# Optimization experiments

Measured on AMD Instinct MI355X. Metric: run time of the kernel, lower is better.

## Reference

```python
import jax, jax.numpy as jnp
import numpy as np

S = 4096          # number of samples
N_NODES = 2048    # sum nodes in this layer
N_CHILD = 4096    # nodes per child layer
NNZ = 32768       # nonzeros per sparse log-weight matrix


def setup_inputs() -> dict:
    key = jax.random.key(0)
    ks = jax.random.split(key, 8)
    ll0 = jax.random.normal(ks[0], (S, N_CHILD), dtype=jnp.float32)
    ll1 = jax.random.normal(ks[1], (S, N_CHILD), dtype=jnp.float32)
    w0_data = jax.random.normal(ks[2], (NNZ,), dtype=jnp.float32)
    w1_data = jax.random.normal(ks[3], (NNZ,), dtype=jnp.float32)
    w0_rows = jax.random.randint(ks[4], (NNZ,), 0, N_NODES, dtype=jnp.int32)
    w0_cols = jax.random.randint(ks[5], (NNZ,), 0, N_CHILD, dtype=jnp.int32)
    w1_rows = jax.random.randint(ks[6], (NNZ,), 0, N_NODES, dtype=jnp.int32)
    w1_cols = jax.random.randint(ks[7], (NNZ,), 0, N_CHILD, dtype=jnp.int32)
    return {"ll0": ll0, "ll1": ll1,
            "w0_data": w0_data, "w1_data": w1_data,
            "w0_rows": w0_rows, "w0_cols": w0_cols,
            "w1_rows": w1_rows, "w1_cols": w1_cols,
            "n_nodes": N_NODES}


def _sparse_weighted_sum(ll, data, rows, cols, n_nodes):
    # exp(ll) @ exp(W).T for BCOO W with shape (n_nodes, n_child)
    # contrib[s, k] = exp(ll[s, cols[k]]) * exp(data[k]); scatter-add over rows.
    contrib = jnp.exp(ll[:, cols] + data[None, :])  # (S, NNZ)
    return jnp.zeros((ll.shape[0], n_nodes), dtype=ll.dtype).at[:, rows].add(contrib)


def reference(ll0, ll1, w0_data, w1_data, w0_rows, w0_cols, w1_rows, w1_cols, n_nodes):
    # accumulate exp(ll_i) @ exp(W_i).T over child layers
    result = _sparse_weighted_sum(ll0, w0_data, w0_rows, w0_cols, n_nodes)
    result = result + _sparse_weighted_sum(ll1, w1_data, w1_rows, w1_cols, n_nodes)
    # log normalization constants: log(sum_j exp(concatenated log_weights)[i, j])
    z = jnp.zeros((n_nodes,), dtype=result.dtype)
    z = z.at[w0_rows].add(jnp.exp(w0_data))
    z = z.at[w1_rows].add(jnp.exp(w1_data))
    return jnp.log(result) - jnp.log(z)[None, :]
```

## Files before the change

kernel.cpp:

```cpp
#include <hip/hip_runtime.h>
#include <math.h>

#define S 4096
#define N_NODES 2048
#define N_CHILD 4096
#define NNZ 32768
#define NNZ_TOTAL (2 * NNZ)
#define TSM 512
#define TN 8
#define CAP 96
#define LP 516

typedef float f32x2 __attribute__((ext_vector_type(2)));


__global__ __launch_bounds__(256, 8) void prep_kernel(
        const float* __restrict__ ll0, const float* __restrict__ ll1,
        const float* __restrict__ w0d, const float* __restrict__ w1d,
        const int* __restrict__ w0r, const int* __restrict__ w0c,
        const int* __restrict__ w1r, const int* __restrict__ w1c,
        unsigned char* __restrict__ ET, int2* __restrict__ ent,
        int* __restrict__ counts) {
    __shared__ unsigned int tile[256 * 5];
    int t = threadIdx.x;
    int b = blockIdx.x;
    if (b < 256) {
        int k = b * 256 + t;
        int row, col; float w;
        if (k < NNZ) { row = w0r[k]; col = w0c[k]; w = w0d[k]; }
        else { int kk = k - NNZ; row = w1r[kk]; col = w1c[kk] + N_CHILD; w = w1d[kk]; }
        int pos = atomicAdd(&counts[row], 1);
        if (pos < CAP)
            ent[row * CAP + pos] = make_int2(col, __float_as_int(__expf(w)));
        return;
    }
    int bt = b - 256;
    int slice = bt & 7;
    int ssub = (bt >> 3) & 31;
    int ct = (bt >> 8) & 15;
    int z = (bt >> 12) & 1;
    int s0 = slice * 512 + ssub * 16;
    int c0 = ct * 256;
    const float* ll = z ? ll1 : ll0;
    int wave = t >> 6, lane = t & 63;
    const float* p = ll + (size_t)(s0 + wave * 4) * N_CHILD + c0 + lane * 4;
    float4 a0 = *(const float4*)(p);
    float4 a1 = *(const float4*)(p + N_CHILD);
    float4 a2 = *(const float4*)(p + 2 * N_CHILD);
    float4 a3 = *(const float4*)(p + 3 * N_CHILD);
#pragma unroll
    for (int k = 0; k < 4; ++k) {
        float e0 = __expf(((const float*)&a0)[k]);
        float e1 = __expf(((const float*)&a1)[k]);
        float e2 = __expf(((const float*)&a2)[k]);
        float e3 = __expf(((const float*)&a3)[k]);
        unsigned int wlo = (unsigned int)__builtin_amdgcn_cvt_pk_fp8_f32(
            e0, e1, 0, false);
        unsigned int wfull = (unsigned int)__builtin_amdgcn_cvt_pk_fp8_f32(
            e2, e3, (int)wlo, true);
        tile[(k * 64 + lane) * 5 + wave] = wfull;
    }
    __syncthreads();
    unsigned int d0 = tile[t * 5 + 0];
    unsigned int d1 = tile[t * 5 + 1];
    unsigned int d2 = tile[t * 5 + 2];
    unsigned int d3 = tile[t * 5 + 3];
    int c = (t & 63) * 4 + (t >> 6);
    unsigned char* dst = ET + (size_t)(z * N_CHILD + c0 + c) * S + s0;
    *(uint4*)dst = make_uint4(d0, d1, d2, d3);
}


static __device__ inline void fma16(uint4 x, f32x2 w2, f32x2* a2) {
#pragma unroll
    for (int q = 0; q < 4; ++q) {
        unsigned int word = (q == 0) ? x.x : (q == 1) ? x.y : (q == 2) ? x.z : x.w;
        f32x2 lo = __builtin_amdgcn_cvt_pk_f32_fp8(word, false);
        f32x2 hi = __builtin_amdgcn_cvt_pk_f32_fp8(word, true);
        a2[q * 2 + 0] = lo * w2 + a2[q * 2 + 0];
        a2[q * 2 + 1] = hi * w2 + a2[q * 2 + 1];
    }
}

__global__ __launch_bounds__(256, 8) void main_kernel(
        const unsigned char* __restrict__ ET, const int2* __restrict__ ent,
        const int* __restrict__ counts, float* __restrict__ out) {
    __shared__ float lds[TN * LP];
    int t = threadIdx.x, wave = t >> 6, lane = t & 63;
    int hs = lane >> 5, sl = lane & 31;
    int slice = blockIdx.x & 7;
    int nb = blockIdx.x >> 3;
    int i0 = nb * TN;
    const unsigned char* ETs = ET + slice * TSM + sl * 16;
    for (int jj = 0; jj < 2; ++jj) {
        int j = wave * 2 + jj;
        int i = i0 + j;
        int cnt = __builtin_amdgcn_readfirstlane(counts[i]);
        if (cnt > CAP) cnt = CAP;
        const int2* eb = ent + i * CAP;
        f32x2 a2[8];
#pragma unroll
        for (int u = 0; u < 8; ++u) a2[u] = (f32x2){0.f, 0.f};
        float z = 0.f;
        int n = (cnt + 1 - hs) >> 1;
        int t2 = 0;
        for (; t2 + 1 < n; t2 += 2) {
            int2 e0 = eb[hs + 2 * t2];
            int2 e1 = eb[hs + 2 * t2 + 2];
            uint4 x0 = *(const uint4*)(ETs + (size_t)e0.x * S);
            uint4 x1 = *(const uint4*)(ETs + (size_t)e1.x * S);
            float w0 = __uint_as_float(e0.y);
            float w1 = __uint_as_float(e1.y);
            f32x2 w02 = {w0, w0};
            f32x2 w12 = {w1, w1};
            fma16(x0, w02, a2);
            fma16(x1, w12, a2);
            z += w0 + w1;
        }
        if (t2 < n) {
            int2 e0 = eb[hs + 2 * t2];
            uint4 x0 = *(const uint4*)(ETs + (size_t)e0.x * S);
            float w0 = __uint_as_float(e0.y);
            f32x2 w02 = {w0, w0};
            fma16(x0, w02, a2);
            z += w0;
        }
        float fl[16];
#pragma unroll
        for (int u = 0; u < 8; ++u) { fl[2 * u] = a2[u].x; fl[2 * u + 1] = a2[u].y; }
#pragma unroll
        for (int u = 0; u < 16; ++u) fl[u] += __shfl_xor(fl[u], 32);
        z += __shfl_xor(z, 32);
        float lz = __logf(z);
        float r[8];
#pragma unroll
        for (int u = 0; u < 8; ++u) {
            float sel = hs ? fl[8 + u] : fl[u];
            r[u] = __logf(sel) - lz;
        }
        float* dstl = &lds[j * LP + sl * 16 + hs * 8];
        *(float4*)(dstl)     = make_float4(r[0], r[1], r[2], r[3]);
        *(float4*)(dstl + 4) = make_float4(r[4], r[5], r[6], r[7]);
    }
    __syncthreads();
    float* obase = out + (size_t)slice * TSM * N_NODES + i0;
#pragma unroll
    for (int q = 0; q < 8; ++q) {
        int elem = (t + 256 * q) * 2;
        int s_l = elem >> 3;
        int i_l = elem & 7;
        float2 v;
        v.x = lds[i_l * LP + s_l];
        v.y = lds[(i_l + 1) * LP + s_l];
        *(float2*)&obase[(size_t)s_l * N_NODES + i_l] = v;
    }
}


extern "C" void kernel_launch(void* const* d_in, const int* in_sizes, int n_in,
                              void* d_out, int out_size, void* d_ws, size_t ws_size,
                              hipStream_t stream) {
    const float* ll0 = (const float*)d_in[0];
    const float* ll1 = (const float*)d_in[1];
    const float* w0d = (const float*)d_in[2];
    const float* w1d = (const float*)d_in[3];
    const int*   w0r = (const int*)d_in[4];
    const int*   w0c = (const int*)d_in[5];
    const int*   w1r = (const int*)d_in[6];
    const int*   w1c = (const int*)d_in[7];
    float* out = (float*)d_out;

    unsigned char* ET = (unsigned char*)d_ws;
    int2* ent   = (int2*)(ET + (size_t)2 * N_CHILD * S);
    int*  counts = (int*)(ent + (size_t)N_NODES * CAP);

    hipMemsetAsync(counts, 0, sizeof(int) * N_NODES, stream);
    prep_kernel<<<256 + 8192, 256, 0, stream>>>(ll0, ll1, w0d, w1d, w0r, w0c,
                                                w1r, w1c, ET, ent, counts);
    main_kernel<<<(N_NODES / TN) * (S / TSM), 256, 0, stream>>>(ET, ent, counts, out);
}
```

Before: 225.5 us.

## Fuse prep and main kernels into one launch with per-slice atomic flags

Merges the sparse bucketing, the fp8 exp-transpose and the sparse weighted-sum into a single 2048-block kernel. Blocks first do their share of the transpose (and bucketing for one group), then signal per-slice counters and spin-wait only on the slice they consume. This removes a kernel boundary and lets slices proceed as soon as their data is ready. It relies on all blocks being co-resident; otherwise the spin-wait can deadlock, and the polling adds overhead.

New measurement: 694.5 us. 208% more time.

```diff
diff --git a/kernel.cpp b/kernel.cpp
--- a/kernel.cpp
+++ b/kernel.cpp
@@ -5,70 +5,12 @@
 #define N_NODES 2048
 #define N_CHILD 4096
 #define NNZ 32768
-#define NNZ_TOTAL (2 * NNZ)
 #define TSM 512
 #define TN 8
 #define CAP 96
 #define LP 516
 
 typedef float f32x2 __attribute__((ext_vector_type(2)));
-
-
-__global__ __launch_bounds__(256, 8) void prep_kernel(
-        const float* __restrict__ ll0, const float* __restrict__ ll1,
-        const float* __restrict__ w0d, const float* __restrict__ w1d,
-        const int* __restrict__ w0r, const int* __restrict__ w0c,
-        const int* __restrict__ w1r, const int* __restrict__ w1c,
-        unsigned char* __restrict__ ET, int2* __restrict__ ent,
-        int* __restrict__ counts) {
-    __shared__ unsigned int tile[256 * 5];
-    int t = threadIdx.x;
-    int b = blockIdx.x;
-    if (b < 256) {
-        int k = b * 256 + t;
-        int row, col; float w;
-        if (k < NNZ) { row = w0r[k]; col = w0c[k]; w = w0d[k]; }
-        else { int kk = k - NNZ; row = w1r[kk]; col = w1c[kk] + N_CHILD; w = w1d[kk]; }
-        int pos = atomicAdd(&counts[row], 1);
-        if (pos < CAP)
-            ent[row * CAP + pos] = make_int2(col, __float_as_int(__expf(w)));
-        return;
-    }
-    int bt = b - 256;
-    int slice = bt & 7;
-    int ssub = (bt >> 3) & 31;
-    int ct = (bt >> 8) & 15;
-    int z = (bt >> 12) & 1;
-    int s0 = slice * 512 + ssub * 16;
-    int c0 = ct * 256;
-    const float* ll = z ? ll1 : ll0;
-    int wave = t >> 6, lane = t & 63;
-    const float* p = ll + (size_t)(s0 + wave * 4) * N_CHILD + c0 + lane * 4;
-    float4 a0 = *(const float4*)(p);
-    float4 a1 = *(const float4*)(p + N_CHILD);
-    float4 a2 = *(const float4*)(p + 2 * N_CHILD);
-    float4 a3 = *(const float4*)(p + 3 * N_CHILD);
-#pragma unroll
-    for (int k = 0; k < 4; ++k) {
-        float e0 = __expf(((const float*)&a0)[k]);
-        float e1 = __expf(((const float*)&a1)[k]);
-        float e2 = __expf(((const float*)&a2)[k]);
-        float e3 = __expf(((const float*)&a3)[k]);
-        unsigned int wlo = (unsigned int)__builtin_amdgcn_cvt_pk_fp8_f32(
-            e0, e1, 0, false);
-        unsigned int wfull = (unsigned int)__builtin_amdgcn_cvt_pk_fp8_f32(
-            e2, e3, (int)wlo, true);
-        tile[(k * 64 + lane) * 5 + wave] = wfull;
-    }
-    __syncthreads();
-    unsigned int d0 = tile[t * 5 + 0];
-    unsigned int d1 = tile[t * 5 + 1];
-    unsigned int d2 = tile[t * 5 + 2];
-    unsigned int d3 = tile[t * 5 + 3];
-    int c = (t & 63) * 4 + (t >> 6);
-    unsigned char* dst = ET + (size_t)(z * N_CHILD + c0 + c) * S + s0;
-    *(uint4*)dst = make_uint4(d0, d1, d2, d3);
-}
 
 
 static __device__ inline void fma16(uint4 x, f32x2 w2, f32x2* a2) {
@@ -82,16 +24,87 @@
     }
 }
 
-__global__ __launch_bounds__(256, 8) void main_kernel(
-        const unsigned char* __restrict__ ET, const int2* __restrict__ ent,
-        const int* __restrict__ counts, float* __restrict__ out) {
-    __shared__ float lds[TN * LP];
-    int t = threadIdx.x, wave = t >> 6, lane = t & 63;
+__global__ __launch_bounds__(256, 8) void fused_kernel(
+        const float* __restrict__ ll0, const float* __restrict__ ll1,
+        const float* __restrict__ w0d, const float* __restrict__ w1d,
+        const int* __restrict__ w0r, const int* __restrict__ w0c,
+        const int* __restrict__ w1r, const int* __restrict__ w1c,
+        unsigned char* __restrict__ ET, int2* __restrict__ ent,
+        int* __restrict__ counts, int* __restrict__ sync_,
+        float* __restrict__ out) {
+    __shared__ float smem[TN * LP];
+    unsigned int* tile = (unsigned int*)smem;
+    int t = threadIdx.x, b = blockIdx.x;
+    int wave = t >> 6, lane = t & 63;
+    int sigma = b >> 8;
+
+    if (sigma == 7) {
+        int k = (b - 1792) * 256 + t;
+        int row, col; float w;
+        if (k < NNZ) { row = w0r[k]; col = w0c[k]; w = w0d[k]; }
+        else { int kk = k - NNZ; row = w1r[kk]; col = w1c[kk] + N_CHILD; w = w1d[kk]; }
+        int pos = atomicAdd(&counts[row], 1);
+        if (pos < CAP)
+            ent[row * CAP + pos] = make_int2(col, __float_as_int(__expf(w)));
+        __syncthreads();
+        if (t == 0) {
+            __threadfence();
+            __hip_atomic_fetch_add(&sync_[0], 1, __ATOMIC_RELEASE,
+                                   __HIP_MEMORY_SCOPE_AGENT);
+        }
+    }
+
+    int r = b & 255;
+    int z = r & 1, ct = (r >> 1) & 15, sgroup = r >> 5;
+    int c0 = ct * 256;
+    const float* ll = z ? ll1 : ll0;
+    for (int j = 0; j < 4; ++j) {
+        int s0 = sigma * 512 + sgroup * 64 + j * 16;
+        const float* p = ll + (size_t)(s0 + wave * 4) * N_CHILD + c0 + lane * 4;
+        float4 a0 = *(const float4*)(p);
+        float4 a1 = *(const float4*)(p + N_CHILD);
+        float4 a2 = *(const float4*)(p + 2 * N_CHILD);
+        float4 a3 = *(const float4*)(p + 3 * N_CHILD);
+#pragma unroll
+        for (int k = 0; k < 4; ++k) {
+            float e0 = __expf(((const float*)&a0)[k]);
+            float e1 = __expf(((const float*)&a1)[k]);
+            float e2 = __expf(((const float*)&a2)[k]);
+            float e3 = __expf(((const float*)&a3)[k]);
+            unsigned int wlo = (unsigned int)__builtin_amdgcn_cvt_pk_fp8_f32(
+                e0, e1, 0, false);
+            unsigned int wfull = (unsigned int)__builtin_amdgcn_cvt_pk_fp8_f32(
+                e2, e3, (int)wlo, true);
+            tile[(k * 64 + lane) * 5 + wave] = wfull;
+        }
+        __syncthreads();
+        unsigned int d0 = tile[t * 5 + 0];
+        unsigned int d1 = tile[t * 5 + 1];
+        unsigned int d2 = tile[t * 5 + 2];
+        unsigned int d3 = tile[t * 5 + 3];
+        int c = (t & 63) * 4 + (t >> 6);
+        unsigned char* dst = ET + (size_t)(z * N_CHILD + c0 + c) * S + s0;
+        *(uint4*)dst = make_uint4(d0, d1, d2, d3);
+        __syncthreads();
+    }
+    if (t == 0) {
+        __threadfence();
+        __hip_atomic_fetch_add(&sync_[1 + sigma], 1, __ATOMIC_RELEASE,
+                               __HIP_MEMORY_SCOPE_AGENT);
+    }
+
+    int s_m = b & 7, nb = b >> 3, i0 = nb * TN;
+    if (t == 0) {
+        while (__hip_atomic_load(&sync_[0], __ATOMIC_ACQUIRE,
+                                 __HIP_MEMORY_SCOPE_AGENT) < 256)
+            __builtin_amdgcn_s_sleep(2);
+        while (__hip_atomic_load(&sync_[1 + s_m], __ATOMIC_ACQUIRE,
+                                 __HIP_MEMORY_SCOPE_AGENT) < 256)
+            __builtin_amdgcn_s_sleep(2);
+    }
+    __syncthreads();
     int hs = lane >> 5, sl = lane & 31;
-    int slice = blockIdx.x & 7;
-    int nb = blockIdx.x >> 3;
-    int i0 = nb * TN;
-    const unsigned char* ETs = ET + slice * TSM + sl * 16;
+    const unsigned char* ETs = ET + s_m * TSM + sl * 16;
     for (int jj = 0; jj < 2; ++jj) {
         int j = wave * 2 + jj;
         int i = i0 + j;
@@ -101,7 +114,7 @@
         f32x2 a2[8];
 #pragma unroll
         for (int u = 0; u < 8; ++u) a2[u] = (f32x2){0.f, 0.f};
-        float z = 0.f;
+        float zz = 0.f;
         int n = (cnt + 1 - hs) >> 1;
         int t2 = 0;
         for (; t2 + 1 < n; t2 += 2) {
@@ -115,7 +128,7 @@
             f32x2 w12 = {w1, w1};
             fma16(x0, w02, a2);
             fma16(x1, w12, a2);
-            z += w0 + w1;
+            zz += w0 + w1;
         }
         if (t2 < n) {
             int2 e0 = eb[hs + 2 * t2];
@@ -123,35 +136,35 @@
             float w0 = __uint_as_float(e0.y);
             f32x2 w02 = {w0, w0};
             fma16(x0, w02, a2);
-            z += w0;
+            zz += w0;
         }
         float fl[16];
 #pragma unroll
         for (int u = 0; u < 8; ++u) { fl[2 * u] = a2[u].x; fl[2 * u + 1] = a2[u].y; }
 #pragma unroll
         for (int u = 0; u < 16; ++u) fl[u] += __shfl_xor(fl[u], 32);
-        z += __shfl_xor(z, 32);
-        float lz = __logf(z);
-        float r[8];
+        zz += __shfl_xor(zz, 32);
+        float lz = __logf(zz);
+        float rr[8];
 #pragma unroll
         for (int u = 0; u < 8; ++u) {
             float sel = hs ? fl[8 + u] : fl[u];
-            r[u] = __logf(sel) - lz;
+            rr[u] = __logf(sel) - lz;
         }
-        float* dstl = &lds[j * LP + sl * 16 + hs * 8];
-        *(float4*)(dstl)     = make_float4(r[0], r[1], r[2], r[3]);
-        *(float4*)(dstl + 4) = make_float4(r[4], r[5], r[6], r[7]);
+        float* dstl = &smem[j * LP + sl * 16 + hs * 8];
+        *(float4*)(dstl)     = make_float4(rr[0], rr[1], rr[2], rr[3]);
+        *(float4*)(dstl + 4) = make_float4(rr[4], rr[5], rr[6], rr[7]);
     }
     __syncthreads();
-    float* obase = out + (size_t)slice * TSM * N_NODES + i0;
+    float* obase = out + (size_t)s_m * TSM * N_NODES + i0;
 #pragma unroll
     for (int q = 0; q < 8; ++q) {
         int elem = (t + 256 * q) * 2;
         int s_l = elem >> 3;
         int i_l = elem & 7;
         float2 v;
-        v.x = lds[i_l * LP + s_l];
-        v.y = lds[(i_l + 1) * LP + s_l];
+        v.x = smem[i_l * LP + s_l];
+        v.y = smem[(i_l + 1) * LP + s_l];
         *(float2*)&obase[(size_t)s_l * N_NODES + i_l] = v;
     }
 }
@@ -173,9 +186,9 @@
     unsigned char* ET = (unsigned char*)d_ws;
     int2* ent   = (int2*)(ET + (size_t)2 * N_CHILD * S);
     int*  counts = (int*)(ent + (size_t)N_NODES * CAP);
+    int*  sync_  = counts + N_NODES;
 
-    hipMemsetAsync(counts, 0, sizeof(int) * N_NODES, stream);
-    prep_kernel<<<256 + 8192, 256, 0, stream>>>(ll0, ll1, w0d, w1d, w0r, w0c,
-                                                w1r, w1c, ET, ent, counts);
-    main_kernel<<<(N_NODES / TN) * (S / TSM), 256, 0, stream>>>(ET, ent, counts, out);
+    hipMemsetAsync(counts, 0, sizeof(int) * (N_NODES + 16), stream);
+    fused_kernel<<<2048, 256, 0, stream>>>(ll0, ll1, w0d, w1d, w0r, w0c,
+                                           w1r, w1c, ET, ent, counts, sync_, out);
 }
```
